# Kernel tuning notes

Measured on AMD Instinct MI355X. Metric: run time of the kernel, lower is better.

The kernel has to match this reference:

```python
import jax, jax.numpy as jnp
import numpy as np

B, D = 500000, 128
UNITS, STACK, NPRED = 4, 12, 2
EPS = 1e-3  # Keras BatchNormalization default epsilon


def setup_inputs() -> dict:
    key = jax.random.key(0)
    ks = jax.random.split(key, 2 * STACK + 4)
    inp = {"x": jax.random.normal(ks[0], (B, D), dtype=jnp.float32)}
    # 12 dense weights with growing input width D + 4*i
    for i in range(STACK):
        inp[f"w{i}"] = jax.random.normal(ks[1 + i], (D + UNITS * i, UNITS), dtype=jnp.float32) * 0.1
    inp["gamma"] = 1.0 + 0.1 * jax.random.normal(ks[STACK + 1], (STACK, UNITS), dtype=jnp.float32)
    inp["beta"] = 0.1 * jax.random.normal(ks[STACK + 2], (STACK, UNITS), dtype=jnp.float32)
    inp["mean"] = 0.1 * jax.random.normal(ks[STACK + 3], (STACK, UNITS), dtype=jnp.float32)
    inp["var"] = 0.5 + jax.random.uniform(ks[2 * STACK], (STACK, UNITS), dtype=jnp.float32)
    inp["wf"] = jax.random.normal(ks[2 * STACK + 1], (D + UNITS * STACK, NPRED), dtype=jnp.float32) * 0.1
    inp["bf"] = jnp.zeros((NPRED,), dtype=jnp.float32)
    return inp


def reference(x, w0, w1, w2, w3, w4, w5, w6, w7, w8, w9, w10, w11,
              gamma, beta, mean, var, wf, bf):
    ws = [w0, w1, w2, w3, w4, w5, w6, w7, w8, w9, w10, w11]
    h = x
    for i in range(STACK):
        y = h @ ws[i]  # [B, 4]
        # inference-mode BatchNorm, fused scale/shift
        scale = gamma[i] * jax.lax.rsqrt(var[i] + EPS)
        y = jax.nn.relu(y * scale + (beta[i] - mean[i] * scale))
        h = jnp.concatenate([y, h], axis=-1)  # width grows by 4
    logits = h @ wf + bf  # [B, 2]
    return jax.nn.softmax(logits, axis=-1)
```

## Files before the change

### kernel.cpp

```cpp
#include <hip/hip_runtime.h>

#define NROWS 500000
#define DD 128
#define NSTACK 12
#define BNEPS 1e-3f
#define NCOL 50
#define TRS 51
#define NTILES ((NROWS + 255) / 256)
#define PERSIST 768

typedef float  v2f    __attribute__((ext_vector_type(2)));
typedef float  v4f    __attribute__((ext_vector_type(4)));
typedef float  f32x4  __attribute__((ext_vector_type(4)));
typedef __bf16 bf16x8 __attribute__((ext_vector_type(8)));

__device__ __forceinline__ unsigned short f2bf_rn(float f) {
    unsigned u = __float_as_uint(f);
    return (unsigned short)((u + 0x7FFFu + ((u >> 16) & 1u)) >> 16);
}


__global__ void prep_kernel(
    const float* __restrict__ w0,  const float* __restrict__ w1,
    const float* __restrict__ w2,  const float* __restrict__ w3,
    const float* __restrict__ w4,  const float* __restrict__ w5,
    const float* __restrict__ w6,  const float* __restrict__ w7,
    const float* __restrict__ w8,  const float* __restrict__ w9,
    const float* __restrict__ w10, const float* __restrict__ w11,
    const float* __restrict__ gamma_, const float* __restrict__ beta_,
    const float* __restrict__ mean_,  const float* __restrict__ var_,
    const float* __restrict__ wf,     const float* __restrict__ bfv,
    unsigned short* __restrict__ frag, float* __restrict__ sc,
    float* __restrict__ sh, float* __restrict__ bf2)
{
    const float* ws[NSTACK] = {w0,w1,w2,w3,w4,w5,w6,w7,w8,w9,w10,w11};
    const int f    = blockIdx.x * 256 + threadIdx.x;
    const int j    = f & 7;
    const int lane = (f >> 3) & 63;
    const int nt   = (f >> 9) & 3;
    const int kt   = f >> 11;
    const int k    = kt * 32 + (lane >> 4) * 8 + j;
    const int n    = nt * 16 + (lane & 15);

    float val = 0.f;
    if (n < 48) {
        const int i = n >> 2, u = n & 3;
        val = ws[i][16 * i + 4 * k + u];
    } else if (n < NCOL) {
        val = wf[96 + 2 * k + (n - 48)];
    }
    frag[f] = f2bf_rn(val);

    if (blockIdx.x == 0) {
        if (threadIdx.x < 48) {
            const float s = gamma_[threadIdx.x] * __frsqrt_rn(var_[threadIdx.x] + BNEPS);
            sc[threadIdx.x] = s;
            sh[threadIdx.x] = beta_[threadIdx.x] - mean_[threadIdx.x] * s;
        }
        if (threadIdx.x < 2) bf2[threadIdx.x] = bfv[threadIdx.x];
    }
}

__global__ __launch_bounds__(256, 3) void predict_kernel(
    const float* __restrict__ x,
    const float* __restrict__ w0,  const float* __restrict__ w1,
    const float* __restrict__ w2,  const float* __restrict__ w3,
    const float* __restrict__ w4,  const float* __restrict__ w5,
    const float* __restrict__ w6,  const float* __restrict__ w7,
    const float* __restrict__ w8,  const float* __restrict__ w9,
    const float* __restrict__ w10, const float* __restrict__ w11,
    const float* __restrict__ wf,
    const unsigned short* __restrict__ frag,
    const float* __restrict__ SCg, const float* __restrict__ SHg,
    const float* __restrict__ BFg,
    float* __restrict__ out)
{
    __shared__ __align__(16) float trow[256 * TRS];

    const int tid  = threadIdx.x;
    const int lane = tid & 63;
    const int wv   = tid >> 6;
    const int m = lane & 15;
    const int q = lane >> 4;
    float* tr = &trow[wv * 64 * TRS];
    const float* myT = &trow[(wv * 64 + lane) * TRS];
    const float* ws[NSTACK] = {w0,w1,w2,w3,w4,w5,w6,w7,w8,w9,w10,w11};

    int T = blockIdx.x;
    int rowbase = T * 256 + wv * 64;

    const float* arow[4];
#pragma unroll
    for (int mt = 0; mt < 4; ++mt) {
        int r = rowbase + mt * 16 + m;
        if (r > NROWS - 1) r = NROWS - 1;
        arow[mt] = x + (size_t)r * DD + q * 8;
    }

    v4f pf0[4], pf1[4];
#pragma unroll
    for (int mt = 0; mt < 4; ++mt) {
        pf0[mt] = *(const v4f*)(arow[mt]);
        pf1[mt] = *(const v4f*)(arow[mt] + 4);
    }

    for (;;) {
        f32x4 acc[4][4];
#pragma unroll
        for (int mt = 0; mt < 4; ++mt)
#pragma unroll
            for (int nt = 0; nt < 4; ++nt) acc[mt][nt] = (f32x4){0.f, 0.f, 0.f, 0.f};

        {
            bf16x8 bfrag[4];
#pragma unroll
            for (int nt = 0; nt < 4; ++nt)
                bfrag[nt] = *(const bf16x8*)(frag + ((nt * 64 + lane) << 3));
#pragma unroll
            for (int mt = 0; mt < 4; ++mt) {
                bf16x8 av;
#pragma unroll
                for (int e = 0; e < 4; ++e) {
                    av[e]     = (__bf16)pf0[mt][e];
                    av[4 + e] = (__bf16)pf1[mt][e];
                }
#pragma unroll
                for (int nt = 0; nt < 4; ++nt)
                    acc[mt][nt] = __builtin_amdgcn_mfma_f32_16x16x32_bf16(
                        av, bfrag[nt], acc[mt][nt], 0, 0, 0);
            }
        }

#pragma unroll
        for (int kt = 1; kt < 4; ++kt) {
            bf16x8 bfrag[4];
#pragma unroll
            for (int nt = 0; nt < 4; ++nt)
                bfrag[nt] = *(const bf16x8*)(frag + (((kt * 4 + nt) * 64 + lane) << 3));
#pragma unroll
            for (int mt = 0; mt < 4; ++mt) {
                const v4f a0 = *(const v4f*)(arow[mt] + kt * 32);
                const v4f a1 = *(const v4f*)(arow[mt] + kt * 32 + 4);
                bf16x8 av;
#pragma unroll
                for (int e = 0; e < 4; ++e) {
                    av[e]     = (__bf16)a0[e];
                    av[4 + e] = (__bf16)a1[e];
                }
#pragma unroll
                for (int nt = 0; nt < 4; ++nt)
                    acc[mt][nt] = __builtin_amdgcn_mfma_f32_16x16x32_bf16(
                        av, bfrag[nt], acc[mt][nt], 0, 0, 0);
            }
        }

#pragma unroll
        for (int mt = 0; mt < 4; ++mt)
#pragma unroll
            for (int nt = 0; nt < 4; ++nt) {
                const int c = nt * 16 + m;
                if (c < NCOL) {
#pragma unroll
                    for (int r = 0; r < 4; ++r)
                        tr[(mt * 16 + q * 4 + r) * TRS + c] = acc[mt][nt][r];
                }
            }

        const int Tn = T + PERSIST;
        const bool more = (Tn < NTILES);
        if (more) {
            const int rb_n = Tn * 256 + wv * 64;
#pragma unroll
            for (int mt = 0; mt < 4; ++mt) {
                int r = rb_n + mt * 16 + m;
                if (r > NROWS - 1) r = NROWS - 1;
                arow[mt] = x + (size_t)r * DD + q * 8;
            }
#pragma unroll
            for (int mt = 0; mt < 4; ++mt) {
                pf0[mt] = *(const v4f*)(arow[mt]);
                pf1[mt] = *(const v4f*)(arow[mt] + 4);
            }
        }

        v2f y2[NSTACK * 2];
#pragma unroll
        for (int i = 0; i < NSTACK; ++i) {
            v2f a01 = *(const v2f*)(myT + 4 * i);
            v2f a23 = *(const v2f*)(myT + 4 * i + 2);
            const float* wsi = ws[i];
#pragma unroll
            for (int mr = 0; mr < 4 * i; ++mr) {
                const int yi = (i - 1 - (mr >> 2)) * 4 + (mr & 3);
                const float hvs = y2[yi >> 1][yi & 1];
                const v2f hv2 = {hvs, hvs};
                a01 += hv2 * (*(const v2f*)(wsi + 4 * mr));
                a23 += hv2 * (*(const v2f*)(wsi + 4 * mr + 2));
            }
            const v2f sc01 = *(const v2f*)(SCg + 4 * i);
            const v2f sc23 = *(const v2f*)(SCg + 4 * i + 2);
            const v2f sh01 = *(const v2f*)(SHg + 4 * i);
            const v2f sh23 = *(const v2f*)(SHg + 4 * i + 2);
            v2f r01 = a01 * sc01 + sh01;
            v2f r23 = a23 * sc23 + sh23;
            r01.x = fmaxf(r01.x, 0.f); r01.y = fmaxf(r01.y, 0.f);
            r23.x = fmaxf(r23.x, 0.f); r23.y = fmaxf(r23.y, 0.f);
            y2[2 * i]     = r01;
            y2[2 * i + 1] = r23;
        }

        v2f l01 = *(const v2f*)(myT + 48) + *(const v2f*)BFg;
#pragma unroll
        for (int mr = 0; mr < 48; ++mr) {
            const int yi = (11 - (mr >> 2)) * 4 + (mr & 3);
            const float hvs = y2[yi >> 1][yi & 1];
            const v2f hv2 = {hvs, hvs};
            l01 += hv2 * (*(const v2f*)(wf + 2 * mr));
        }

        const float mx = fmaxf(l01.x, l01.y);
        const float e0 = __expf(l01.x - mx);
        const float e1 = __expf(l01.y - mx);
        const float inv = 1.0f / (e0 + e1);

        const int row = rowbase + lane;
        if (row < NROWS)
            *(v2f*)(out + (size_t)row * 2) = (v2f){e0 * inv, e1 * inv};

        if (!more) break;
        T = Tn;
        rowbase = Tn * 256 + wv * 64;
    }
}

extern "C" void kernel_launch(void* const* d_in, const int* in_sizes, int n_in,
                              void* d_out, int out_size, void* d_ws, size_t ws_size,
                              hipStream_t stream) {
    const float* x   = (const float*)d_in[0];
    const float* w0  = (const float*)d_in[1];
    const float* w1  = (const float*)d_in[2];
    const float* w2  = (const float*)d_in[3];
    const float* w3  = (const float*)d_in[4];
    const float* w4  = (const float*)d_in[5];
    const float* w5  = (const float*)d_in[6];
    const float* w6  = (const float*)d_in[7];
    const float* w7  = (const float*)d_in[8];
    const float* w8  = (const float*)d_in[9];
    const float* w9  = (const float*)d_in[10];
    const float* w10 = (const float*)d_in[11];
    const float* w11 = (const float*)d_in[12];
    const float* gm  = (const float*)d_in[13];
    const float* bt  = (const float*)d_in[14];
    const float* mn  = (const float*)d_in[15];
    const float* vr  = (const float*)d_in[16];
    const float* wf  = (const float*)d_in[17];
    const float* bf  = (const float*)d_in[18];
    float* out = (float*)d_out;

    unsigned short* frag = (unsigned short*)d_ws;
    float* SCg = (float*)((char*)d_ws + 16384);
    float* SHg = (float*)((char*)d_ws + 16576);
    float* BFg = (float*)((char*)d_ws + 16768);

    hipLaunchKernelGGL(prep_kernel, dim3(32), dim3(256), 0, stream,
                       w0, w1, w2, w3, w4, w5, w6, w7, w8, w9, w10, w11,
                       gm, bt, mn, vr, wf, bf, frag, SCg, SHg, BFg);

    hipLaunchKernelGGL(predict_kernel, dim3(PERSIST), dim3(256), 0, stream,
                       x, w0, w1, w2, w3, w4, w5, w6, w7, w8, w9, w10, w11,
                       wf, frag, SCg, SHg, BFg, out);
}
```

Baseline: 415.4 us.

## Replace static block-stride tiling with per-wave dynamic work stealing via atomic counter

Each wave now owns a 64-row tile and fetches its next tile through a global atomicAdd counter, which prep_kernel initializes. Previously each 256-thread block advanced by a fixed stride of PERSIST tiles. The aim is to balance load across waves and CUs and cut tail imbalance in the persistent kernel. The cost is one atomic per wave per tile, which may contend. Consecutive rows are also no longer grouped per block.

```diff
diff --git a/kernel.cpp b/kernel.cpp
--- a/kernel.cpp
+++ b/kernel.cpp
@@ -6,8 +6,9 @@
 #define BNEPS 1e-3f
 #define NCOL 50
 #define TRS 51
-#define NTILES ((NROWS + 255) / 256)
 #define PERSIST 768
+#define NT_WAVE ((NROWS + 63) / 64)
+#define CTR_INIT (PERSIST * 4)
 
 typedef float  v2f    __attribute__((ext_vector_type(2)));
 typedef float  v4f    __attribute__((ext_vector_type(4)));
@@ -31,7 +32,7 @@
     const float* __restrict__ mean_,  const float* __restrict__ var_,
     const float* __restrict__ wf,     const float* __restrict__ bfv,
     unsigned short* __restrict__ frag, float* __restrict__ sc,
-    float* __restrict__ sh, float* __restrict__ bf2)
+    float* __restrict__ sh, float* __restrict__ bf2, int* __restrict__ ctr)
 {
     const float* ws[NSTACK] = {w0,w1,w2,w3,w4,w5,w6,w7,w8,w9,w10,w11};
     const int f    = blockIdx.x * 256 + threadIdx.x;
@@ -58,6 +59,7 @@
             sh[threadIdx.x] = beta_[threadIdx.x] - mean_[threadIdx.x] * s;
         }
         if (threadIdx.x < 2) bf2[threadIdx.x] = bfv[threadIdx.x];
+        if (threadIdx.x == 0) *ctr = CTR_INIT;
     }
 }
 
@@ -72,7 +74,7 @@
     const float* __restrict__ wf,
     const unsigned short* __restrict__ frag,
     const float* __restrict__ SCg, const float* __restrict__ SHg,
-    const float* __restrict__ BFg,
+    const float* __restrict__ BFg, int* __restrict__ ctr,
     float* __restrict__ out)
 {
     __shared__ __align__(16) float trow[256 * TRS];
@@ -86,13 +88,12 @@
     const float* myT = &trow[(wv * 64 + lane) * TRS];
     const float* ws[NSTACK] = {w0,w1,w2,w3,w4,w5,w6,w7,w8,w9,w10,w11};
 
-    int T = blockIdx.x;
-    int rowbase = T * 256 + wv * 64;
+    int T = blockIdx.x * 4 + wv;
 
     const float* arow[4];
 #pragma unroll
     for (int mt = 0; mt < 4; ++mt) {
-        int r = rowbase + mt * 16 + m;
+        int r = T * 64 + mt * 16 + m;
         if (r > NROWS - 1) r = NROWS - 1;
         arow[mt] = x + (size_t)r * DD + q * 8;
     }
@@ -166,13 +167,14 @@
                 }
             }
 
-        const int Tn = T + PERSIST;
-        const bool more = (Tn < NTILES);
+        int Tn;
+        if (lane == 0) Tn = atomicAdd(ctr, 1);
+        Tn = __shfl(Tn, 0);
+        const bool more = (Tn < NT_WAVE);
         if (more) {
-            const int rb_n = Tn * 256 + wv * 64;
-#pragma unroll
-            for (int mt = 0; mt < 4; ++mt) {
-                int r = rb_n + mt * 16 + m;
+#pragma unroll
+            for (int mt = 0; mt < 4; ++mt) {
+                int r = Tn * 64 + mt * 16 + m;
                 if (r > NROWS - 1) r = NROWS - 1;
                 arow[mt] = x + (size_t)r * DD + q * 8;
             }
@@ -223,13 +225,12 @@
         const float e1 = __expf(l01.y - mx);
         const float inv = 1.0f / (e0 + e1);
 
-        const int row = rowbase + lane;
+        const int row = T * 64 + lane;
         if (row < NROWS)
             *(v2f*)(out + (size_t)row * 2) = (v2f){e0 * inv, e1 * inv};
 
         if (!more) break;
         T = Tn;
-        rowbase = Tn * 256 + wv * 64;
     }
 }
 
@@ -261,12 +262,13 @@
     float* SCg = (float*)((char*)d_ws + 16384);
     float* SHg = (float*)((char*)d_ws + 16576);
     float* BFg = (float*)((char*)d_ws + 16768);
+    int*   CTR = (int*)((char*)d_ws + 16784);
 
     hipLaunchKernelGGL(prep_kernel, dim3(32), dim3(256), 0, stream,
                        w0, w1, w2, w3, w4, w5, w6, w7, w8, w9, w10, w11,
-                       gm, bt, mn, vr, wf, bf, frag, SCg, SHg, BFg);
+                       gm, bt, mn, vr, wf, bf, frag, SCg, SHg, BFg, CTR);
 
     hipLaunchKernelGGL(predict_kernel, dim3(PERSIST), dim3(256), 0, stream,
                        x, w0, w1, w2, w3, w4, w5, w6, w7, w8, w9, w10, w11,
-                       wf, frag, SCg, SHg, BFg, out);
-}
+                       wf, frag, SCg, SHg, BFg, CTR, out);
+}
```

Result: slower. 466.6 us (+12.3%).
